# Performance work log

Measured on AMD Instinct MI355X. Metric: run time of the kernel, lower is better.

## Reference

```python
import jax, jax.numpy as jnp
import numpy as np

H, W = 720, 1280
NVIEWS, FEAT, HIDDEN = 30, 8, 64
GRIDS = ((16, 16, 8), (12, 12, 8), (8, 8, 4))  # (grid_X, grid_Y, grid_W) per scale
RGB2GRAY = np.array([0.299, 0.587, 0.114], dtype=np.float32)


def setup_inputs() -> dict:
    key = jax.random.key(0)
    ks = jax.random.split(key, 8)
    inp = {"rgb": jax.random.uniform(ks[0], (H, W, 3), jnp.float32)}
    for i, (gx, gy, gl) in enumerate(GRIDS):
        # grids: (N, C, L, Hg, Wg) per the docstring '(N, 12, L, H, W)'
        inp[f"grids{i}"] = jax.random.normal(ks[1 + i], (NVIEWS, FEAT, gl, gy, gx), jnp.float32) * 0.1
    din = len(GRIDS) * FEAT
    inp["w1"] = jax.random.normal(ks[4], (din, HIDDEN), jnp.float32) / np.sqrt(din)
    inp["w2"] = jax.random.normal(ks[5], (HIDDEN, HIDDEN), jnp.float32) / np.sqrt(HIDDEN)
    inp["w3"] = jax.random.normal(ks[6], (HIDDEN, 12), jnp.float32) / np.sqrt(HIDDEN)
    inp["cam_idx"] = 5
    return inp


def _slice_grid(g, rgb):
    """Trilinear bilateral-grid slicing (grid_sample 3D, align_corners=True).

    g: (C, L, Hg, Wg) grid for one view; rgb: (h, w, 3) in [0,1].
    Guidance z = gray luma; x/y are the normalized [0,1] image meshgrid.
    Returns (h, w, C).
    """
    C, L, Hg, Wg = g.shape
    h, w, _ = rgb.shape
    gray = jnp.clip(rgb @ jnp.asarray(RGB2GRAY, rgb.dtype), 0.0, 1.0)  # (h, w)
    # align_corners=True: normalized coord u in [0,1] -> u * (size - 1)
    x = jnp.broadcast_to(jnp.linspace(0.0, Wg - 1.0, w, dtype=rgb.dtype)[None, :], (h, w))
    y = jnp.broadcast_to(jnp.linspace(0.0, Hg - 1.0, h, dtype=rgb.dtype)[:, None], (h, w))
    z = gray * (L - 1.0)

    x0 = jnp.floor(x).astype(jnp.int32); x1 = jnp.minimum(x0 + 1, Wg - 1)
    y0 = jnp.floor(y).astype(jnp.int32); y1 = jnp.minimum(y0 + 1, Hg - 1)
    z0 = jnp.floor(z).astype(jnp.int32); z1 = jnp.minimum(z0 + 1, L - 1)
    wx, wy, wz = x - x0, y - y0, z - z0  # (h, w)

    def gat(zi, yi, xi):
        return g[:, zi, yi, xi]  # (C, h, w)

    c00 = gat(z0, y0, x0) * (1 - wx) + gat(z0, y0, x1) * wx
    c01 = gat(z0, y1, x0) * (1 - wx) + gat(z0, y1, x1) * wx
    c10 = gat(z1, y0, x0) * (1 - wx) + gat(z1, y0, x1) * wx
    c11 = gat(z1, y1, x0) * (1 - wx) + gat(z1, y1, x1) * wx
    c0 = c00 * (1 - wy) + c01 * wy
    c1 = c10 * (1 - wy) + c11 * wy
    out = c0 * (1 - wz) + c1 * wz  # (C, h, w)
    return jnp.transpose(out, (1, 2, 0))


def reference(rgb, grids0, grids1, grids2, w1, w2, w3, cam_idx):
    h, w, _ = rgb.shape
    feats = jnp.concatenate(
        [_slice_grid(g[cam_idx], rgb) for g in (grids0, grids1, grids2)], axis=-1
    )  # (h, w, 3*FEAT)
    hid = jnp.tanh(feats @ w1)
    hid = jnp.tanh(hid @ w2)
    out = hid @ w3  # (h, w, 12)
    return out.reshape(1, h, w, 3, 4)
```

## Files before the change

kernel.cpp:

```cpp
#include <hip/hip_runtime.h>
#include <hip/hip_bf16.h>

#define H_IMG 720
#define W_IMG 1280
#define NPIX (H_IMG * W_IMG)

typedef __attribute__((ext_vector_type(4))) float f32x4;
typedef __attribute__((ext_vector_type(8))) short short8;
typedef __attribute__((ext_vector_type(4))) short short4v;
typedef __attribute__((ext_vector_type(4))) uint u32x4;
typedef _Float16 h8 __attribute__((ext_vector_type(8)));

#define WPACK_BYTES (14 * 64 * 16)
#define GP0_OFF WPACK_BYTES
#define GP0_N (16 * 16 * 8 * 8)
#define GP1_OFF (GP0_OFF + GP0_N * 2)
#define GP1_N (12 * 12 * 8 * 8)
#define GP2_OFF (GP1_OFF + GP1_N * 2)
#define GP2_N (8 * 8 * 4 * 8)

#define HSTR 68

#define KSCALE 2.885390081777927f

__device__ __forceinline__ uint pkh(float a, float b) {
  auto t = __builtin_amdgcn_cvt_pkrtz(a, b);
  return __builtin_bit_cast(uint, t);
}

__device__ __forceinline__ float tanhu(float u) {
  float e2 = __builtin_amdgcn_exp2f(u);
  float r = __builtin_amdgcn_rcpf(e2 + 1.f);
  return fmaf(-2.f, r, 1.f);
}

__device__ __forceinline__ uint2 tanh4(f32x4 u) {
  return make_uint2(pkh(tanhu(u[0]), tanhu(u[1])), pkh(tanhu(u[2]), tanhu(u[3])));
}

__global__ __launch_bounds__(256) void prep_kernel(
    const float* __restrict__ g0, const float* __restrict__ g1, const float* __restrict__ g2,
    const float* __restrict__ w1, const float* __restrict__ w2, const float* __restrict__ w3,
    const int* __restrict__ cam, void* __restrict__ ws) {
  ushort* wpack = (ushort*)ws;
  ushort* gp0 = (ushort*)((char*)ws + GP0_OFF);
  ushort* gp1 = (ushort*)((char*)ws + GP1_OFF);
  ushort* gp2 = (ushort*)((char*)ws + GP2_OFF);
  const int ci = cam[0];
  const int tid = blockIdx.x * 256 + threadIdx.x;
  const int nth = gridDim.x * 256;

  for (int e = tid; e < GP0_N; e += nth) {
    int c = e & 7; int t = e >> 3; int z = t & 7; t >>= 3; int x = t & 15; int y = t >> 4;
    _Float16 hv = (_Float16)g0[ci * GP0_N + ((c * 8 + z) * 16 + y) * 16 + x];
    gp0[e] = __builtin_bit_cast(ushort, hv);
  }
  for (int e = tid; e < GP1_N; e += nth) {
    int c = e & 7; int t = e >> 3; int z = t & 7; t >>= 3; int x = t % 12; int y = t / 12;
    _Float16 hv = (_Float16)g1[ci * GP1_N + ((c * 8 + z) * 12 + y) * 12 + x];
    gp1[e] = __builtin_bit_cast(ushort, hv);
  }
  for (int e = tid; e < GP2_N; e += nth) {
    int c = e & 7; int t = e >> 3; int z = t & 3; t >>= 2; int x = t & 7; int y = t >> 3;
    _Float16 hv = (_Float16)g2[ci * GP2_N + ((c * 4 + z) * 8 + y) * 8 + x];
    gp2[e] = __builtin_bit_cast(ushort, hv);
  }

  for (int fl = tid; fl < 14 * 64; fl += nth) {
    int f = fl >> 6, lane = fl & 63;
    int g = lane >> 4, r = lane & 15;
    ushort* dh = wpack + fl * 8;
#pragma unroll
    for (int j = 0; j < 8; ++j) {
      float v = 0.f;
      if (f < 4) {
        int k = 8 * g + j, n = r + 16 * f;
        if (k < 24) v = w1[k * 64 + n] * KSCALE;
      } else if (f < 12) {
        int q = f - 4, ks = q >> 2, mt = q & 3;
        v = w2[(8 * g + j + 32 * ks) * 64 + (r + 16 * mt)] * KSCALE;
      } else {
        int ks = f - 12;
        if (r < 12) v = w3[(8 * g + j + 32 * ks) * 12 + r];
      }
      _Float16 hv = (_Float16)v;
      dh[j] = __builtin_bit_cast(ushort, hv);
    }
  }
}

template <int WG, int HG, int LG>
__device__ __forceinline__ h8 slice_h8(const h8* __restrict__ gp,
                                       int row, int col, float gray) {
  float x = (float)col * ((float)(WG - 1) / (float)(W_IMG - 1));
  float y = (float)row * ((float)(HG - 1) / (float)(H_IMG - 1));
  float z = gray * (float)(LG - 1);
  int x0 = (int)x, y0 = (int)y, z0 = (int)z;
  int x1 = min(x0 + 1, WG - 1), y1 = min(y0 + 1, HG - 1), z1 = min(z0 + 1, LG - 1);
  _Float16 wx = (_Float16)(x - (float)x0);
  _Float16 wy = (_Float16)(y - (float)y0);
  _Float16 wz = (_Float16)(z - (float)z0);
  h8 wx8 = {wx, wx, wx, wx, wx, wx, wx, wx};
  h8 wy8 = {wy, wy, wy, wy, wy, wy, wy, wy};
  h8 wz8 = {wz, wz, wz, wz, wz, wz, wz, wz};

  const h8* p00 = gp + (y0 * WG + x0) * LG;
  const h8* p01 = gp + (y0 * WG + x1) * LG;
  const h8* p10 = gp + (y1 * WG + x0) * LG;
  const h8* p11 = gp + (y1 * WG + x1) * LG;

  h8 a00 = p00[z0], a01 = p01[z0], a10 = p10[z0], a11 = p11[z0];
  h8 b00 = p00[z1], b01 = p01[z1], b10 = p10[z1], b11 = p11[z1];

  h8 xa = a00 + wx8 * (a01 - a00);
  h8 xb = a10 + wx8 * (a11 - a10);
  h8 ya = xa + wy8 * (xb - xa);
  h8 xc = b00 + wx8 * (b01 - b00);
  h8 xd = b10 + wx8 * (b11 - b10);
  h8 yb = xc + wy8 * (xd - xc);
  return ya + wz8 * (yb - ya);
}

__global__ __launch_bounds__(64, 4) void msnbat_kernel(
    const float* __restrict__ rgb, const void* __restrict__ ws, float* __restrict__ out) {
  __shared__ ushort W[64 * HSTR];
  uint* Wu = (uint*)W;

  const h8* wp = (const h8*)ws;
  const h8* gp0 = (const h8*)((const char*)ws + GP0_OFF);
  const h8* gp1 = (const h8*)((const char*)ws + GP1_OFF);
  const h8* gp2 = (const h8*)((const char*)ws + GP2_OFF);

  const int lane = threadIdx.x;
  const int g = lane >> 4, r = lane & 15;
  const int pixbase = blockIdx.x * 64;
  const int p = pixbase + lane;
  const int row = p / W_IMG;
  const int col = p - row * W_IMG;

  const float rr = rgb[p * 3 + 0], gg = rgb[p * 3 + 1], bb = rgb[p * 3 + 2];
  const float gray = fminf(fmaxf(rr * 0.299f + gg * 0.587f + bb * 0.114f, 0.f), 1.f);

  h8 f0 = slice_h8<16, 16, 8>(gp0, row, col, gray);
  h8 f1 = slice_h8<12, 12, 8>(gp1, row, col, gray);
  h8 f2 = slice_h8<8, 8, 4>(gp2, row, col, gray);

  {
    const int ub = lane * (HSTR / 2);
    u32x4 u0 = __builtin_bit_cast(u32x4, f0);
    u32x4 u1 = __builtin_bit_cast(u32x4, f1);
    u32x4 u2 = __builtin_bit_cast(u32x4, f2);
    *(uint2*)&Wu[ub + 0] = make_uint2(u0[0], u0[1]);
    *(uint2*)&Wu[ub + 2] = make_uint2(u0[2], u0[3]);
    *(uint2*)&Wu[ub + 4] = make_uint2(u1[0], u1[1]);
    *(uint2*)&Wu[ub + 6] = make_uint2(u1[2], u1[3]);
    *(uint2*)&Wu[ub + 8] = make_uint2(u2[0], u2[1]);
    *(uint2*)&Wu[ub + 10] = make_uint2(u2[2], u2[3]);
  }

  const h8 zero8 = (h8){0, 0, 0, 0, 0, 0, 0, 0};

  h8 B1[4];
#pragma unroll
  for (int nt = 0; nt < 4; ++nt) {
    short4v lo = *(short4v*)&W[(r + 16 * nt) * HSTR + 8 * g];
    short4v hi = *(short4v*)&W[(r + 16 * nt) * HSTR + 8 * g + 4];
    short8 s = __builtin_shufflevector(lo, hi, 0, 1, 2, 3, 4, 5, 6, 7);
    B1[nt] = (g < 3) ? __builtin_bit_cast(h8, s) : zero8;
  }

  {
    f32x4 a1[4][4];
#pragma unroll
    for (int mt = 0; mt < 4; ++mt)
#pragma unroll
      for (int nt = 0; nt < 4; ++nt) a1[mt][nt] = (f32x4){0.f, 0.f, 0.f, 0.f};
#pragma unroll
    for (int mt = 0; mt < 4; ++mt) {
      h8 A = wp[mt * 64 + lane];
#pragma unroll
      for (int nt = 0; nt < 4; ++nt)
        a1[mt][nt] = __builtin_amdgcn_mfma_f32_16x16x32_f16(A, B1[nt], a1[mt][nt], 0, 0, 0);
    }
#pragma unroll
    for (int mt = 0; mt < 4; ++mt)
#pragma unroll
      for (int nt = 0; nt < 4; ++nt)
        *(uint2*)&Wu[(16 * nt + r) * (HSTR / 2) + 8 * mt + 2 * g] = tanh4(a1[mt][nt]);
  }

  h8 B2[2][4];
#pragma unroll
  for (int ks = 0; ks < 2; ++ks)
#pragma unroll
    for (int nt = 0; nt < 4; ++nt) {
      short4v lo = *(short4v*)&W[(16 * nt + r) * HSTR + 32 * ks + 8 * g];
      short4v hi = *(short4v*)&W[(16 * nt + r) * HSTR + 32 * ks + 8 * g + 4];
      short8 s = __builtin_shufflevector(lo, hi, 0, 1, 2, 3, 4, 5, 6, 7);
      B2[ks][nt] = __builtin_bit_cast(h8, s);
    }

  {
    f32x4 a2[4][4];
#pragma unroll
    for (int mt = 0; mt < 4; ++mt)
#pragma unroll
      for (int nt = 0; nt < 4; ++nt) a2[mt][nt] = (f32x4){0.f, 0.f, 0.f, 0.f};
#pragma unroll
    for (int ks = 0; ks < 2; ++ks)
#pragma unroll
      for (int mt = 0; mt < 4; ++mt) {
        h8 A = wp[(4 + ks * 4 + mt) * 64 + lane];
#pragma unroll
        for (int nt = 0; nt < 4; ++nt)
          a2[mt][nt] = __builtin_amdgcn_mfma_f32_16x16x32_f16(A, B2[ks][nt], a2[mt][nt], 0, 0, 0);
      }
#pragma unroll
    for (int mt = 0; mt < 4; ++mt)
#pragma unroll
      for (int nt = 0; nt < 4; ++nt)
        *(uint2*)&Wu[(16 * nt + r) * (HSTR / 2) + 8 * mt + 2 * g] = tanh4(a2[mt][nt]);
  }

  f32x4 acc3[4];
#pragma unroll
  for (int nt = 0; nt < 4; ++nt) acc3[nt] = (f32x4){0.f, 0.f, 0.f, 0.f};
#pragma unroll
  for (int ks = 0; ks < 2; ++ks) {
    h8 A = wp[(12 + ks) * 64 + lane];
#pragma unroll
    for (int nt = 0; nt < 4; ++nt) {
      short4v lo = *(short4v*)&W[(16 * nt + r) * HSTR + 32 * ks + 8 * g];
      short4v hi = *(short4v*)&W[(16 * nt + r) * HSTR + 32 * ks + 8 * g + 4];
      short8 s = __builtin_shufflevector(lo, hi, 0, 1, 2, 3, 4, 5, 6, 7);
      h8 B = __builtin_bit_cast(h8, s);
      acc3[nt] = __builtin_amdgcn_mfma_f32_16x16x32_f16(A, B, acc3[nt], 0, 0, 0);
    }
  }

  if (g < 3) {
#pragma unroll
    for (int nt = 0; nt < 4; ++nt) {
      int pix = pixbase + 16 * nt + r;
      *(f32x4*)(out + pix * 12 + 4 * g) = acc3[nt];
    }
  }
}

extern "C" void kernel_launch(void* const* d_in, const int* in_sizes, int n_in,
                              void* d_out, int out_size, void* d_ws, size_t ws_size,
                              hipStream_t stream) {
  const float* rgb = (const float*)d_in[0];
  const float* g0 = (const float*)d_in[1];
  const float* g1 = (const float*)d_in[2];
  const float* g2 = (const float*)d_in[3];
  const float* w1 = (const float*)d_in[4];
  const float* w2 = (const float*)d_in[5];
  const float* w3 = (const float*)d_in[6];
  const int* cam = (const int*)d_in[7];
  float* out = (float*)d_out;

  hipLaunchKernelGGL(prep_kernel, dim3(64), dim3(256), 0, stream,
                     g0, g1, g2, w1, w2, w3, cam, d_ws);
  hipLaunchKernelGGL(msnbat_kernel, dim3(NPIX / 64), dim3(64), 0, stream,
                     rgb, d_ws, out);
}
```

Before: 51.63 us.

## Process two 64-pixel tiles per wavefront to reuse weight fragments

Each single-wave block now handles 128 pixels as two tiles with separate LDS buffers. Each loaded weight A fragment feeds MFMAs for both tiles, which halves global weight loads per pixel. Layer-2 is reordered to compute per output tile. The change also gives more independent MFMA work to hide latency, at the cost of higher register pressure (two accumulator sets), double the LDS per block, and half as many blocks.

```diff
diff --git a/kernel.cpp b/kernel.cpp
--- a/kernel.cpp
+++ b/kernel.cpp
@@ -123,9 +123,7 @@
 
 __global__ __launch_bounds__(64, 4) void msnbat_kernel(
     const float* __restrict__ rgb, const void* __restrict__ ws, float* __restrict__ out) {
-  __shared__ ushort W[64 * HSTR];
-  uint* Wu = (uint*)W;
-
+  __shared__ ushort W[2][64 * HSTR];
   const h8* wp = (const h8*)ws;
   const h8* gp0 = (const h8*)((const char*)ws + GP0_OFF);
   const h8* gp1 = (const h8*)((const char*)ws + GP1_OFF);
@@ -133,19 +131,27 @@
 
   const int lane = threadIdx.x;
   const int g = lane >> 4, r = lane & 15;
-  const int pixbase = blockIdx.x * 64;
-  const int p = pixbase + lane;
-  const int row = p / W_IMG;
-  const int col = p - row * W_IMG;
-
-  const float rr = rgb[p * 3 + 0], gg = rgb[p * 3 + 1], bb = rgb[p * 3 + 2];
-  const float gray = fminf(fmaxf(rr * 0.299f + gg * 0.587f + bb * 0.114f, 0.f), 1.f);
-
-  h8 f0 = slice_h8<16, 16, 8>(gp0, row, col, gray);
-  h8 f1 = slice_h8<12, 12, 8>(gp1, row, col, gray);
-  h8 f2 = slice_h8<8, 8, 4>(gp2, row, col, gray);
-
-  {
+  const int pixbase = blockIdx.x * 128;
+
+  float gray[2];
+#pragma unroll
+  for (int t = 0; t < 2; ++t) {
+    int p = pixbase + 64 * t + lane;
+    int prow = p / W_IMG;
+    float rr = rgb[p * 3 + 0], gg = rgb[p * 3 + 1], bb = rgb[p * 3 + 2];
+    gray[t] = fminf(fmaxf(rr * 0.299f + gg * 0.587f + bb * 0.114f, 0.f), 1.f);
+    (void)prow;
+  }
+
+#pragma unroll
+  for (int t = 0; t < 2; ++t) {
+    int p = pixbase + 64 * t + lane;
+    int prow = p / W_IMG;
+    int pcol = p - prow * W_IMG;
+    h8 f0 = slice_h8<16, 16, 8>(gp0, prow, pcol, gray[t]);
+    h8 f1 = slice_h8<12, 12, 8>(gp1, prow, pcol, gray[t]);
+    h8 f2 = slice_h8<8, 8, 4>(gp2, prow, pcol, gray[t]);
+    uint* Wu = (uint*)W[t];
     const int ub = lane * (HSTR / 2);
     u32x4 u0 = __builtin_bit_cast(u32x4, f0);
     u32x4 u1 = __builtin_bit_cast(u32x4, f1);
@@ -160,90 +166,107 @@
 
   const h8 zero8 = (h8){0, 0, 0, 0, 0, 0, 0, 0};
 
-  h8 B1[4];
-#pragma unroll
-  for (int nt = 0; nt < 4; ++nt) {
-    short4v lo = *(short4v*)&W[(r + 16 * nt) * HSTR + 8 * g];
-    short4v hi = *(short4v*)&W[(r + 16 * nt) * HSTR + 8 * g + 4];
-    short8 s = __builtin_shufflevector(lo, hi, 0, 1, 2, 3, 4, 5, 6, 7);
-    B1[nt] = (g < 3) ? __builtin_bit_cast(h8, s) : zero8;
-  }
-
-  {
-    f32x4 a1[4][4];
-#pragma unroll
-    for (int mt = 0; mt < 4; ++mt)
-#pragma unroll
-      for (int nt = 0; nt < 4; ++nt) a1[mt][nt] = (f32x4){0.f, 0.f, 0.f, 0.f};
-#pragma unroll
-    for (int mt = 0; mt < 4; ++mt) {
-      h8 A = wp[mt * 64 + lane];
-#pragma unroll
-      for (int nt = 0; nt < 4; ++nt)
-        a1[mt][nt] = __builtin_amdgcn_mfma_f32_16x16x32_f16(A, B1[nt], a1[mt][nt], 0, 0, 0);
-    }
-#pragma unroll
-    for (int mt = 0; mt < 4; ++mt)
-#pragma unroll
-      for (int nt = 0; nt < 4; ++nt)
-        *(uint2*)&Wu[(16 * nt + r) * (HSTR / 2) + 8 * mt + 2 * g] = tanh4(a1[mt][nt]);
-  }
-
-  h8 B2[2][4];
-#pragma unroll
-  for (int ks = 0; ks < 2; ++ks)
+  h8 B1[2][4];
+#pragma unroll
+  for (int t = 0; t < 2; ++t)
 #pragma unroll
     for (int nt = 0; nt < 4; ++nt) {
-      short4v lo = *(short4v*)&W[(16 * nt + r) * HSTR + 32 * ks + 8 * g];
-      short4v hi = *(short4v*)&W[(16 * nt + r) * HSTR + 32 * ks + 8 * g + 4];
+      short4v lo = *(short4v*)&W[t][(r + 16 * nt) * HSTR + 8 * g];
+      short4v hi = *(short4v*)&W[t][(r + 16 * nt) * HSTR + 8 * g + 4];
       short8 s = __builtin_shufflevector(lo, hi, 0, 1, 2, 3, 4, 5, 6, 7);
-      B2[ks][nt] = __builtin_bit_cast(h8, s);
-    }
-
-  {
-    f32x4 a2[4][4];
-#pragma unroll
-    for (int mt = 0; mt < 4; ++mt)
-#pragma unroll
-      for (int nt = 0; nt < 4; ++nt) a2[mt][nt] = (f32x4){0.f, 0.f, 0.f, 0.f};
+      B1[t][nt] = (g < 3) ? __builtin_bit_cast(h8, s) : zero8;
+    }
+
+#pragma unroll
+  for (int mt = 0; mt < 4; ++mt) {
+    h8 A = wp[mt * 64 + lane];
+    f32x4 a[2][4];
+#pragma unroll
+    for (int t = 0; t < 2; ++t)
+#pragma unroll
+      for (int nt = 0; nt < 4; ++nt) a[t][nt] = (f32x4){0.f, 0.f, 0.f, 0.f};
+#pragma unroll
+    for (int t = 0; t < 2; ++t)
+#pragma unroll
+      for (int nt = 0; nt < 4; ++nt)
+        a[t][nt] = __builtin_amdgcn_mfma_f32_16x16x32_f16(A, B1[t][nt], a[t][nt], 0, 0, 0);
+#pragma unroll
+    for (int t = 0; t < 2; ++t) {
+      uint* Wu = (uint*)W[t];
+#pragma unroll
+      for (int nt = 0; nt < 4; ++nt)
+        *(uint2*)&Wu[(16 * nt + r) * (HSTR / 2) + 8 * mt + 2 * g] = tanh4(a[t][nt]);
+    }
+  }
+
+  h8 B2[2][2][4];
+#pragma unroll
+  for (int t = 0; t < 2; ++t)
 #pragma unroll
     for (int ks = 0; ks < 2; ++ks)
 #pragma unroll
-      for (int mt = 0; mt < 4; ++mt) {
-        h8 A = wp[(4 + ks * 4 + mt) * 64 + lane];
-#pragma unroll
-        for (int nt = 0; nt < 4; ++nt)
-          a2[mt][nt] = __builtin_amdgcn_mfma_f32_16x16x32_f16(A, B2[ks][nt], a2[mt][nt], 0, 0, 0);
-      }
-#pragma unroll
-    for (int mt = 0; mt < 4; ++mt)
-#pragma unroll
-      for (int nt = 0; nt < 4; ++nt)
-        *(uint2*)&Wu[(16 * nt + r) * (HSTR / 2) + 8 * mt + 2 * g] = tanh4(a2[mt][nt]);
-  }
-
-  f32x4 acc3[4];
-#pragma unroll
-  for (int nt = 0; nt < 4; ++nt) acc3[nt] = (f32x4){0.f, 0.f, 0.f, 0.f};
+      for (int nt = 0; nt < 4; ++nt) {
+        short4v lo = *(short4v*)&W[t][(16 * nt + r) * HSTR + 32 * ks + 8 * g];
+        short4v hi = *(short4v*)&W[t][(16 * nt + r) * HSTR + 32 * ks + 8 * g + 4];
+        short8 s = __builtin_shufflevector(lo, hi, 0, 1, 2, 3, 4, 5, 6, 7);
+        B2[t][ks][nt] = __builtin_bit_cast(h8, s);
+      }
+
+#pragma unroll
+  for (int mt = 0; mt < 4; ++mt) {
+    h8 A0 = wp[(4 + mt) * 64 + lane];
+    h8 A1 = wp[(8 + mt) * 64 + lane];
+    f32x4 a[2][4];
+#pragma unroll
+    for (int t = 0; t < 2; ++t)
+#pragma unroll
+      for (int nt = 0; nt < 4; ++nt) a[t][nt] = (f32x4){0.f, 0.f, 0.f, 0.f};
+#pragma unroll
+    for (int t = 0; t < 2; ++t) {
+#pragma unroll
+      for (int nt = 0; nt < 4; ++nt)
+        a[t][nt] = __builtin_amdgcn_mfma_f32_16x16x32_f16(A0, B2[t][0][nt], a[t][nt], 0, 0, 0);
+#pragma unroll
+      for (int nt = 0; nt < 4; ++nt)
+        a[t][nt] = __builtin_amdgcn_mfma_f32_16x16x32_f16(A1, B2[t][1][nt], a[t][nt], 0, 0, 0);
+    }
+#pragma unroll
+    for (int t = 0; t < 2; ++t) {
+      uint* Wu = (uint*)W[t];
+#pragma unroll
+      for (int nt = 0; nt < 4; ++nt)
+        *(uint2*)&Wu[(16 * nt + r) * (HSTR / 2) + 8 * mt + 2 * g] = tanh4(a[t][nt]);
+    }
+  }
+
+  f32x4 acc3[2][4];
+#pragma unroll
+  for (int t = 0; t < 2; ++t)
+#pragma unroll
+    for (int nt = 0; nt < 4; ++nt) acc3[t][nt] = (f32x4){0.f, 0.f, 0.f, 0.f};
 #pragma unroll
   for (int ks = 0; ks < 2; ++ks) {
     h8 A = wp[(12 + ks) * 64 + lane];
 #pragma unroll
-    for (int nt = 0; nt < 4; ++nt) {
-      short4v lo = *(short4v*)&W[(16 * nt + r) * HSTR + 32 * ks + 8 * g];
-      short4v hi = *(short4v*)&W[(16 * nt + r) * HSTR + 32 * ks + 8 * g + 4];
-      short8 s = __builtin_shufflevector(lo, hi, 0, 1, 2, 3, 4, 5, 6, 7);
-      h8 B = __builtin_bit_cast(h8, s);
-      acc3[nt] = __builtin_amdgcn_mfma_f32_16x16x32_f16(A, B, acc3[nt], 0, 0, 0);
-    }
+    for (int t = 0; t < 2; ++t)
+#pragma unroll
+      for (int nt = 0; nt < 4; ++nt) {
+        short4v lo = *(short4v*)&W[t][(16 * nt + r) * HSTR + 32 * ks + 8 * g];
+        short4v hi = *(short4v*)&W[t][(16 * nt + r) * HSTR + 32 * ks + 8 * g + 4];
+        short8 s = __builtin_shufflevector(lo, hi, 0, 1, 2, 3, 4, 5, 6, 7);
+        h8 B = __builtin_bit_cast(h8, s);
+        acc3[t][nt] = __builtin_amdgcn_mfma_f32_16x16x32_f16(A, B, acc3[t][nt], 0, 0, 0);
+      }
   }
 
   if (g < 3) {
 #pragma unroll
-    for (int nt = 0; nt < 4; ++nt) {
-      int pix = pixbase + 16 * nt + r;
-      *(f32x4*)(out + pix * 12 + 4 * g) = acc3[nt];
-    }
+    for (int t = 0; t < 2; ++t)
+#pragma unroll
+      for (int nt = 0; nt < 4; ++nt) {
+        int pix = pixbase + 64 * t + 16 * nt + r;
+        *(f32x4*)(out + pix * 12 + 4 * g) = acc3[t][nt];
+      }
   }
 }
 
@@ -262,6 +285,6 @@
 
   hipLaunchKernelGGL(prep_kernel, dim3(64), dim3(256), 0, stream,
                      g0, g1, g2, w1, w2, w3, cam, d_ws);
-  hipLaunchKernelGGL(msnbat_kernel, dim3(NPIX / 64), dim3(64), 0, stream,
+  hipLaunchKernelGGL(msnbat_kernel, dim3(NPIX / 128), dim3(64), 0, stream,
                      rgb, d_ws, out);
 }
```

Result: slower. 61.56 us (+19.2%).
